# Performance work log

Hardware: AMD Instinct MI355X
Metric: run time of the kernel (lower is better)

The kernel has to match this reference:

```python
import jax, jax.numpy as jnp
import numpy as np

# Dimensions: T time steps, B sequences, F input features, H hidden width, S=1 state size
T, B, F = 4096, 128, 1
H = 256
S = 1
DT = 1.0  # init kwarg dt


def setup_inputs() -> dict:
    key = jax.random.key(0)
    k = jax.random.split(key, 4)
    return {
        "x": jax.random.normal(k[0], (T, B, F), jnp.float32),
        # derivative-network MLP params: input = concat(state, input sample)
        "W1": jax.random.normal(k[1], (S + F, H), jnp.float32) * (1.0 / np.sqrt(S + F)),
        "b1": jnp.zeros((H,), jnp.float32),
        "W2": jax.random.normal(k[2], (H, H), jnp.float32) * (1.0 / np.sqrt(H)),
        "b2": jnp.zeros((H,), jnp.float32),
        "W3": jax.random.normal(k[3], (H, S), jnp.float32) * (1.0 / np.sqrt(H)),
        "b3": jnp.zeros((S,), jnp.float32),
    }


def reference(x, W1, b1, W2, b2, W3, b3):
    """Forward-Euler ODE integration over the time axis of x.

    x: (T, B, F). Returns trajectory of the scalar state, shape (T, B, 1),
    where traj[0] is the zero initial state (odeint returns values at the
    requested time points, starting with the initial value).
    """
    Bsz = x.shape[1]
    y0 = jnp.zeros((Bsz, S), x.dtype)

    def mlp(y, xt):  # derivative network f(t, y): (B,S),(B,F) -> (B,S)
        inp = jnp.concatenate([y, xt], axis=-1)          # (B, S+F)
        h = jnp.tanh(inp @ W1 + b1)                      # (B, H)
        h = jnp.tanh(h @ W2 + b2)                        # (B, H)
        return h @ W3 + b3                               # (B, S)

    def step(y, xt):
        y_next = y + DT * mlp(y, xt)                     # forward Euler
        return y_next, y                                 # emit state at t_n

    _, traj = jax.lax.scan(step, y0, x)                  # traj: (T, B, S)
    return traj
```

## Files before the change

kernel.cpp:

```cpp
#include <hip/hip_runtime.h>

#define T_STEPS 4096
#define BATCH   128
#define HID     256

typedef float f4 __attribute__((ext_vector_type(4)));

__device__ __forceinline__ float fast_tanh(float z) {
    float e = __expf(2.0f * z);
    return 1.0f - 2.0f / (e + 1.0f);
}

__device__ __forceinline__ float rlane(float v, int l) {
    return __uint_as_float(__builtin_amdgcn_readlane(__float_as_uint(v), l));
}

template <int CTRL, int ROW_MASK>
__device__ __forceinline__ float dpp_add(float x) {
    int s = __builtin_amdgcn_update_dpp(0, __float_as_int(x), CTRL, ROW_MASK, 0xf, false);
    return x + __int_as_float(s);
}

#define RPT16(M) M(0) M(1) M(2) M(3) M(4) M(5) M(6) M(7) \
                 M(8) M(9) M(10) M(11) M(12) M(13) M(14) M(15)

__global__ __launch_bounds__(1024, 4)
void odenet_kernel(const float* __restrict__ x,
                   const float* __restrict__ W1, const float* __restrict__ b1,
                   const float* __restrict__ W2, const float* __restrict__ b2,
                   const float* __restrict__ W3, const float* __restrict__ b3,
                   float* __restrict__ out)
{
    const int b = blockIdx.x;
    const int t = threadIdx.x;
    const int w = t >> 6;
    const int l = t & 63;
    const int k = 16 * w + (l & 15);

    __shared__ float x_lds[T_STEPS];
    __shared__ float part[16][HID];
    __shared__ __align__(16) float red[4];

    for (int i = t; i < T_STEPS; i += 1024) x_lds[i] = x[i * BATCH + b];

    #define DECLQ(i) \
        f4 wq##i = *(const f4*)(W2 + (16*w + (i)) * HID + 4*l); \
        asm volatile("" : "+v"(wq##i));
    RPT16(DECLQ)

    const float w1a = W1[k];
    const float w1b = W1[HID + k];
    const float b1v = b1[k];

    const float b2v = (t < 256) ? b2[t] : 0.f;
    const float w3v = (t < 256) ? W3[t] : 0.f;
    const float b3v = b3[0];

    float y = 0.0f;
    __syncthreads();

    #pragma unroll 1
    for (int n = 0; n < T_STEPS; ++n) {
        if (t == 1023) out[n * BATCH + b] = y;

        const float xt = x_lds[n];
        const float h  = fast_tanh(fmaf(y, w1a, fmaf(xt, w1b, b1v)));

        f4 acc = {0.f, 0.f, 0.f, 0.f};
        #define STEPK(i) { const float s = rlane(h, i); acc += s * wq##i; }
        RPT16(STEPK)
        *(f4*)(&part[w][4 * l]) = acc;
        __syncthreads();

        if (t < 256) {
            float s0 = 0.f, s1 = 0.f, s2 = 0.f, s3 = 0.f;
            #pragma unroll
            for (int p = 0; p < 4; ++p) {
                s0 += part[4*p + 0][t];
                s1 += part[4*p + 1][t];
                s2 += part[4*p + 2][t];
                s3 += part[4*p + 3][t];
            }
            float h2 = fast_tanh(((s0 + s1) + (s2 + s3)) + b2v);
            float p  = h2 * w3v;
            p = dpp_add<0x111, 0xf>(p);
            p = dpp_add<0x112, 0xf>(p);
            p = dpp_add<0x114, 0xf>(p);
            p = dpp_add<0x118, 0xf>(p);
            p = dpp_add<0x142, 0xa>(p);
            p = dpp_add<0x143, 0xc>(p);
            if (l == 63) red[w] = p;
        }
        __syncthreads();

        f4 r = *(const f4*)red;
        y += ((r.x + r.y) + (r.z + r.w)) + b3v;
    }
}

extern "C" void kernel_launch(void* const* d_in, const int* in_sizes, int n_in,
                              void* d_out, int out_size, void* d_ws, size_t ws_size,
                              hipStream_t stream) {
    const float* x  = (const float*)d_in[0];
    const float* W1 = (const float*)d_in[1];
    const float* b1 = (const float*)d_in[2];
    const float* W2 = (const float*)d_in[3];
    const float* b2 = (const float*)d_in[4];
    const float* W3 = (const float*)d_in[5];
    const float* b3 = (const float*)d_in[6];
    float* out = (float*)d_out;

    odenet_kernel<<<dim3(BATCH), dim3(1024), 0, stream>>>(x, W1, b1, W2, b2, W3, b3, out);
}
```

Before: 3.577 ms.

## Rewrite recurrent step loop as hand-scheduled inline assembly

```diff
diff --git a/kernel.cpp b/kernel.cpp
--- a/kernel.cpp
+++ b/kernel.cpp
@@ -3,26 +3,6 @@
 #define T_STEPS 4096
 #define BATCH   128
 #define HID     256
-
-typedef float f4 __attribute__((ext_vector_type(4)));
-
-__device__ __forceinline__ float fast_tanh(float z) {
-    float e = __expf(2.0f * z);
-    return 1.0f - 2.0f / (e + 1.0f);
-}
-
-__device__ __forceinline__ float rlane(float v, int l) {
-    return __uint_as_float(__builtin_amdgcn_readlane(__float_as_uint(v), l));
-}
-
-template <int CTRL, int ROW_MASK>
-__device__ __forceinline__ float dpp_add(float x) {
-    int s = __builtin_amdgcn_update_dpp(0, __float_as_int(x), CTRL, ROW_MASK, 0xf, false);
-    return x + __int_as_float(s);
-}
-
-#define RPT16(M) M(0) M(1) M(2) M(3) M(4) M(5) M(6) M(7) \
-                 M(8) M(9) M(10) M(11) M(12) M(13) M(14) M(15)
 
 __global__ __launch_bounds__(1024, 4)
 void odenet_kernel(const float* __restrict__ x,
@@ -37,65 +17,276 @@
     const int l = t & 63;
     const int k = 16 * w + (l & 15);
 
-    __shared__ float x_lds[T_STEPS];
-    __shared__ float part[16][HID];
+    __shared__ __align__(16) float x_lds[T_STEPS];
+    __shared__ __align__(16) float part[16][HID];
     __shared__ __align__(16) float red[4];
 
     for (int i = t; i < T_STEPS; i += 1024) x_lds[i] = x[i * BATCH + b];
-
-    #define DECLQ(i) \
-        f4 wq##i = *(const f4*)(W2 + (16*w + (i)) * HID + 4*l); \
-        asm volatile("" : "+v"(wq##i));
-    RPT16(DECLQ)
 
     const float w1a = W1[k];
     const float w1b = W1[HID + k];
     const float b1v = b1[k];
-
-    const float b2v = (t < 256) ? b2[t] : 0.f;
-    const float w3v = (t < 256) ? W3[t] : 0.f;
+    const int   j   = t & 255;
+    const float b2v = b2[j];
+    const float w3v = W3[j];
     const float b3v = b3[0];
+
+    unsigned x_addr  = (unsigned)(uintptr_t)&x_lds[0];
+    unsigned p_addr  = (unsigned)(uintptr_t)&part[w][4 * l];
+    unsigned c_addr  = (unsigned)(uintptr_t)&part[0][j];
+    unsigned r_addr  = (unsigned)(uintptr_t)&red[w & 3];
+    unsigned rd_addr = (unsigned)(uintptr_t)&red[0];
+    unsigned bp32    = (unsigned)((l ^ 32) << 2);
+    unsigned woff    = (unsigned)(w * 16384 + l * 16);
+    unsigned voff    = (unsigned)(b * 4);
+    unsigned emitf   = (t == 1023) ? 1u : 0u;
+    unsigned cw      = (w < 4) ? 1u : 0u;
+    unsigned long long l0m = 1ull;
 
     float y = 0.0f;
     __syncthreads();
 
-    #pragma unroll 1
-    for (int n = 0; n < T_STEPS; ++n) {
-        if (t == 1023) out[n * BATCH + b] = y;
-
-        const float xt = x_lds[n];
-        const float h  = fast_tanh(fmaf(y, w1a, fmaf(xt, w1b, b1v)));
-
-        f4 acc = {0.f, 0.f, 0.f, 0.f};
-        #define STEPK(i) { const float s = rlane(h, i); acc += s * wq##i; }
-        RPT16(STEPK)
-        *(f4*)(&part[w][4 * l]) = acc;
-        __syncthreads();
-
-        if (t < 256) {
-            float s0 = 0.f, s1 = 0.f, s2 = 0.f, s3 = 0.f;
-            #pragma unroll
-            for (int p = 0; p < 4; ++p) {
-                s0 += part[4*p + 0][t];
-                s1 += part[4*p + 1][t];
-                s2 += part[4*p + 2][t];
-                s3 += part[4*p + 3][t];
-            }
-            float h2 = fast_tanh(((s0 + s1) + (s2 + s3)) + b2v);
-            float p  = h2 * w3v;
-            p = dpp_add<0x111, 0xf>(p);
-            p = dpp_add<0x112, 0xf>(p);
-            p = dpp_add<0x114, 0xf>(p);
-            p = dpp_add<0x118, 0xf>(p);
-            p = dpp_add<0x142, 0xa>(p);
-            p = dpp_add<0x143, 0xc>(p);
-            if (l == 63) red[w] = p;
-        }
-        __syncthreads();
-
-        f4 r = *(const f4*)red;
-        y += ((r.x + r.y) + (r.z + r.w)) + b3v;
-    }
+    asm volatile(
+        "s_mov_b32 s84, 0x1000\n\t"
+        "global_load_dwordx4 v[40:43], %[wo], %[w2]\n\t"
+        "v_add_u32 %[wo], 0x400, %[wo]\n\t"
+        "global_load_dwordx4 v[44:47], %[wo], %[w2]\n\t"
+        "v_add_u32 %[wo], 0x400, %[wo]\n\t"
+        "global_load_dwordx4 v[48:51], %[wo], %[w2]\n\t"
+        "v_add_u32 %[wo], 0x400, %[wo]\n\t"
+        "global_load_dwordx4 v[52:55], %[wo], %[w2]\n\t"
+        "v_add_u32 %[wo], 0x400, %[wo]\n\t"
+        "global_load_dwordx4 v[56:59], %[wo], %[w2]\n\t"
+        "v_add_u32 %[wo], 0x400, %[wo]\n\t"
+        "global_load_dwordx4 v[60:63], %[wo], %[w2]\n\t"
+        "v_add_u32 %[wo], 0x400, %[wo]\n\t"
+        "global_load_dwordx4 v[64:67], %[wo], %[w2]\n\t"
+        "v_add_u32 %[wo], 0x400, %[wo]\n\t"
+        "global_load_dwordx4 v[68:71], %[wo], %[w2]\n\t"
+        "v_add_u32 %[wo], 0x400, %[wo]\n\t"
+        "global_load_dwordx4 v[72:75], %[wo], %[w2]\n\t"
+        "v_add_u32 %[wo], 0x400, %[wo]\n\t"
+        "global_load_dwordx4 v[76:79], %[wo], %[w2]\n\t"
+        "v_add_u32 %[wo], 0x400, %[wo]\n\t"
+        "global_load_dwordx4 v[80:83], %[wo], %[w2]\n\t"
+        "v_add_u32 %[wo], 0x400, %[wo]\n\t"
+        "global_load_dwordx4 v[84:87], %[wo], %[w2]\n\t"
+        "v_add_u32 %[wo], 0x400, %[wo]\n\t"
+        "global_load_dwordx4 v[88:91], %[wo], %[w2]\n\t"
+        "v_add_u32 %[wo], 0x400, %[wo]\n\t"
+        "global_load_dwordx4 v[92:95], %[wo], %[w2]\n\t"
+        "v_add_u32 %[wo], 0x400, %[wo]\n\t"
+        "global_load_dwordx4 v[96:99], %[wo], %[w2]\n\t"
+        "v_add_u32 %[wo], 0x400, %[wo]\n\t"
+        "global_load_dwordx4 v[100:103], %[wo], %[w2]\n\t"
+        "s_waitcnt vmcnt(0)\n\t"
+
+        "Lloop_%=:\n\t"
+        "v_cmp_eq_u32 vcc, 1, %[emf]\n\t"
+        "s_and_saveexec_b64 s[80:81], vcc\n\t"
+        "global_store_dword %[vo], %[y], %[ob]\n\t"
+        "s_mov_b64 exec, -1\n\t"
+        "v_add_u32 %[vo], 0x200, %[vo]\n\t"
+        "ds_read_b32 v32, %[xa]\n\t"
+        "v_add_u32 %[xa], 4, %[xa]\n\t"
+        "v_mov_b32 v33, %[b1]\n\t"
+        "s_waitcnt lgkmcnt(0)\n\t"
+        "v_fmac_f32 v33, v32, %[w1b]\n\t"
+        "v_fmac_f32 v33, %[y], %[w1a]\n\t"
+        "v_mul_f32 v33, 0x4038aa3b, v33\n\t"
+        "v_exp_f32 v33, v33\n\t"
+        "s_nop 0\n\t"
+        "v_add_f32 v33, 1.0, v33\n\t"
+        "v_rcp_f32 v33, v33\n\t"
+        "s_nop 0\n\t"
+        "v_add_f32 v34, v33, v33\n\t"
+        "v_sub_f32 v34, 1.0, v34\n\t"
+        "v_mov_b32 v36, 0\n\t"
+        "v_mov_b32 v37, 0\n\t"
+        "v_mov_b32 v38, 0\n\t"
+        "v_mov_b32 v39, 0\n\t"
+        "v_readlane_b32 s80, v34, 0\n\t"
+        "v_readlane_b32 s81, v34, 1\n\t"
+        "v_readlane_b32 s82, v34, 2\n\t"
+        "v_readlane_b32 s83, v34, 3\n\t"
+        "v_fmac_f32 v36, s80, v40\n\t"
+        "v_fmac_f32 v37, s80, v41\n\t"
+        "v_fmac_f32 v38, s80, v42\n\t"
+        "v_fmac_f32 v39, s80, v43\n\t"
+        "v_readlane_b32 s80, v34, 4\n\t"
+        "v_fmac_f32 v36, s81, v44\n\t"
+        "v_fmac_f32 v37, s81, v45\n\t"
+        "v_fmac_f32 v38, s81, v46\n\t"
+        "v_fmac_f32 v39, s81, v47\n\t"
+        "v_readlane_b32 s81, v34, 5\n\t"
+        "v_fmac_f32 v36, s82, v48\n\t"
+        "v_fmac_f32 v37, s82, v49\n\t"
+        "v_fmac_f32 v38, s82, v50\n\t"
+        "v_fmac_f32 v39, s82, v51\n\t"
+        "v_readlane_b32 s82, v34, 6\n\t"
+        "v_fmac_f32 v36, s83, v52\n\t"
+        "v_fmac_f32 v37, s83, v53\n\t"
+        "v_fmac_f32 v38, s83, v54\n\t"
+        "v_fmac_f32 v39, s83, v55\n\t"
+        "v_readlane_b32 s83, v34, 7\n\t"
+        "v_fmac_f32 v36, s80, v56\n\t"
+        "v_fmac_f32 v37, s80, v57\n\t"
+        "v_fmac_f32 v38, s80, v58\n\t"
+        "v_fmac_f32 v39, s80, v59\n\t"
+        "v_readlane_b32 s80, v34, 8\n\t"
+        "v_fmac_f32 v36, s81, v60\n\t"
+        "v_fmac_f32 v37, s81, v61\n\t"
+        "v_fmac_f32 v38, s81, v62\n\t"
+        "v_fmac_f32 v39, s81, v63\n\t"
+        "v_readlane_b32 s81, v34, 9\n\t"
+        "v_fmac_f32 v36, s82, v64\n\t"
+        "v_fmac_f32 v37, s82, v65\n\t"
+        "v_fmac_f32 v38, s82, v66\n\t"
+        "v_fmac_f32 v39, s82, v67\n\t"
+        "v_readlane_b32 s82, v34, 10\n\t"
+        "v_fmac_f32 v36, s83, v68\n\t"
+        "v_fmac_f32 v37, s83, v69\n\t"
+        "v_fmac_f32 v38, s83, v70\n\t"
+        "v_fmac_f32 v39, s83, v71\n\t"
+        "v_readlane_b32 s83, v34, 11\n\t"
+        "v_fmac_f32 v36, s80, v72\n\t"
+        "v_fmac_f32 v37, s80, v73\n\t"
+        "v_fmac_f32 v38, s80, v74\n\t"
+        "v_fmac_f32 v39, s80, v75\n\t"
+        "v_readlane_b32 s80, v34, 12\n\t"
+        "v_fmac_f32 v36, s81, v76\n\t"
+        "v_fmac_f32 v37, s81, v77\n\t"
+        "v_fmac_f32 v38, s81, v78\n\t"
+        "v_fmac_f32 v39, s81, v79\n\t"
+        "v_readlane_b32 s81, v34, 13\n\t"
+        "v_fmac_f32 v36, s82, v80\n\t"
+        "v_fmac_f32 v37, s82, v81\n\t"
+        "v_fmac_f32 v38, s82, v82\n\t"
+        "v_fmac_f32 v39, s82, v83\n\t"
+        "v_readlane_b32 s82, v34, 14\n\t"
+        "v_fmac_f32 v36, s83, v84\n\t"
+        "v_fmac_f32 v37, s83, v85\n\t"
+        "v_fmac_f32 v38, s83, v86\n\t"
+        "v_fmac_f32 v39, s83, v87\n\t"
+        "v_readlane_b32 s83, v34, 15\n\t"
+        "v_fmac_f32 v36, s80, v88\n\t"
+        "v_fmac_f32 v37, s80, v89\n\t"
+        "v_fmac_f32 v38, s80, v90\n\t"
+        "v_fmac_f32 v39, s80, v91\n\t"
+        "v_fmac_f32 v36, s81, v92\n\t"
+        "v_fmac_f32 v37, s81, v93\n\t"
+        "v_fmac_f32 v38, s81, v94\n\t"
+        "v_fmac_f32 v39, s81, v95\n\t"
+        "v_fmac_f32 v36, s82, v96\n\t"
+        "v_fmac_f32 v37, s82, v97\n\t"
+        "v_fmac_f32 v38, s82, v98\n\t"
+        "v_fmac_f32 v39, s82, v99\n\t"
+        "v_fmac_f32 v36, s83, v100\n\t"
+        "v_fmac_f32 v37, s83, v101\n\t"
+        "v_fmac_f32 v38, s83, v102\n\t"
+        "v_fmac_f32 v39, s83, v103\n\t"
+        "ds_write_b128 %[pa], v[36:39]\n\t"
+        "s_waitcnt lgkmcnt(0)\n\t"
+        "s_barrier\n\t"
+        "v_readfirstlane_b32 s85, %[cw]\n\t"
+        "s_nop 0\n\t"
+        "s_cmp_eq_u32 s85, 0\n\t"
+        "s_cbranch_scc1 Lskip_%=\n\t"
+        "ds_read_b32 v32, %[ca]\n\t"
+        "ds_read_b32 v33, %[ca] offset:1024\n\t"
+        "ds_read_b32 v34, %[ca] offset:2048\n\t"
+        "ds_read_b32 v35, %[ca] offset:3072\n\t"
+        "ds_read_b32 v36, %[ca] offset:4096\n\t"
+        "ds_read_b32 v37, %[ca] offset:5120\n\t"
+        "ds_read_b32 v38, %[ca] offset:6144\n\t"
+        "ds_read_b32 v39, %[ca] offset:7168\n\t"
+        "s_waitcnt lgkmcnt(0)\n\t"
+        "v_add_f32 v32, v32, v33\n\t"
+        "v_add_f32 v34, v34, v35\n\t"
+        "v_add_f32 v36, v36, v37\n\t"
+        "v_add_f32 v38, v38, v39\n\t"
+        "v_add_f32 v32, v32, v34\n\t"
+        "v_add_f32 v36, v36, v38\n\t"
+        "v_add_f32 v32, v32, v36\n\t"
+        "ds_read_b32 v33, %[ca] offset:8192\n\t"
+        "ds_read_b32 v34, %[ca] offset:9216\n\t"
+        "ds_read_b32 v35, %[ca] offset:10240\n\t"
+        "ds_read_b32 v36, %[ca] offset:11264\n\t"
+        "ds_read_b32 v37, %[ca] offset:12288\n\t"
+        "ds_read_b32 v38, %[ca] offset:13312\n\t"
+        "ds_read_b32 v39, %[ca] offset:14336\n\t"
+        "s_waitcnt lgkmcnt(0)\n\t"
+        "v_add_f32 v33, v33, v34\n\t"
+        "v_add_f32 v35, v35, v36\n\t"
+        "v_add_f32 v37, v37, v38\n\t"
+        "v_add_f32 v33, v33, v35\n\t"
+        "v_add_f32 v33, v33, v37\n\t"
+        "v_add_f32 v33, v33, v39\n\t"
+        "v_add_f32 v32, v32, v33\n\t"
+        "ds_read_b32 v34, %[ca] offset:15360\n\t"
+        "s_waitcnt lgkmcnt(0)\n\t"
+        "v_add_f32 v32, v32, v34\n\t"
+        "v_add_f32 v32, %[b2], v32\n\t"
+        "v_mul_f32 v32, 0x4038aa3b, v32\n\t"
+        "v_exp_f32 v32, v32\n\t"
+        "s_nop 0\n\t"
+        "v_add_f32 v32, 1.0, v32\n\t"
+        "v_rcp_f32 v32, v32\n\t"
+        "s_nop 0\n\t"
+        "v_add_f32 v32, v32, v32\n\t"
+        "v_sub_f32 v32, 1.0, v32\n\t"
+        "v_mul_f32 v32, %[w3], v32\n\t"
+        "ds_swizzle_b32 v33, v32 offset:0x041f\n\t"
+        "s_waitcnt lgkmcnt(0)\n\t"
+        "v_add_f32 v32, v32, v33\n\t"
+        "ds_swizzle_b32 v33, v32 offset:0x081f\n\t"
+        "s_waitcnt lgkmcnt(0)\n\t"
+        "v_add_f32 v32, v32, v33\n\t"
+        "ds_swizzle_b32 v33, v32 offset:0x101f\n\t"
+        "s_waitcnt lgkmcnt(0)\n\t"
+        "v_add_f32 v32, v32, v33\n\t"
+        "ds_swizzle_b32 v33, v32 offset:0x201f\n\t"
+        "s_waitcnt lgkmcnt(0)\n\t"
+        "v_add_f32 v32, v32, v33\n\t"
+        "ds_swizzle_b32 v33, v32 offset:0x401f\n\t"
+        "s_waitcnt lgkmcnt(0)\n\t"
+        "v_add_f32 v32, v32, v33\n\t"
+        "ds_bpermute_b32 v33, %[bp], v32\n\t"
+        "s_waitcnt lgkmcnt(0)\n\t"
+        "v_add_f32 v32, v32, v33\n\t"
+        "s_and_saveexec_b64 s[82:83], %[l0]\n\t"
+        "ds_write_b32 %[ra], v32\n\t"
+        "s_mov_b64 exec, -1\n\t"
+        "Lskip_%=:\n\t"
+        "s_waitcnt lgkmcnt(0)\n\t"
+        "s_barrier\n\t"
+        "ds_read_b128 v[32:35], %[rd]\n\t"
+        "s_waitcnt lgkmcnt(0)\n\t"
+        "v_add_f32 v32, v32, v33\n\t"
+        "v_add_f32 v34, v34, v35\n\t"
+        "v_add_f32 v32, v32, v34\n\t"
+        "v_add_f32 v32, %[b3], v32\n\t"
+        "v_add_f32 %[y], %[y], v32\n\t"
+        "s_sub_u32 s84, s84, 1\n\t"
+        "s_cmp_lg_u32 s84, 0\n\t"
+        "s_cbranch_scc1 Lloop_%=\n\t"
+        : [y]"+v"(y), [xa]"+v"(x_addr), [vo]"+v"(voff), [wo]"+v"(woff)
+        : [w2]"s"(W2), [ob]"s"(out), [l0]"s"(l0m),
+          [emf]"v"(emitf), [cw]"v"(cw),
+          [pa]"v"(p_addr), [ca]"v"(c_addr), [ra]"v"(r_addr), [rd]"v"(rd_addr),
+          [bp]"v"(bp32), [w1a]"v"(w1a), [w1b]"v"(w1b), [b1]"v"(b1v),
+          [b2]"v"(b2v), [w3]"v"(w3v), [b3]"v"(b3v)
+        : "memory", "scc", "vcc",
+          "s80","s81","s82","s83","s84","s85",
+          "v32","v33","v34","v35","v36","v37","v38","v39",
+          "v40","v41","v42","v43","v44","v45","v46","v47",
+          "v48","v49","v50","v51","v52","v53","v54","v55",
+          "v56","v57","v58","v59","v60","v61","v62","v63",
+          "v64","v65","v66","v67","v68","v69","v70","v71",
+          "v72","v73","v74","v75","v76","v77","v78","v79",
+          "v80","v81","v82","v83","v84","v85","v86","v87",
+          "v88","v89","v90","v91","v92","v93","v94","v95",
+          "v96","v97","v98","v99","v100","v101","v102","v103");
 }
 
 extern "C" void kernel_launch(void* const* d_in, const int* in_sizes, int n_in,
```

Result: slower. 4.886 ms (+36.6%).
